# Optimization experiments

Measured on AMD Instinct MI355X. Metric: run time of the kernel, lower is better.

Reference implementation:

```python
import jax, jax.numpy as jnp
import numpy as np

SEQ_LEN = 64
WCNT = 50000
EMB = 128
TOPIC = 256
TH = TOPIC // 2          # bidirectional topic GRU hidden (num_layers=1 branch)
KCNT = 16384             # know_length
KE = 64                  # know_emb_size
SH = 512                 # seq_hidden_size
IN_S = 2 * TOPIC + 1     # 'double' score mode GRU input size


def setup_inputs() -> dict:
    key = jax.random.key(0)
    ks = jax.random.split(key, 24)
    rn = lambda k, shape, s=0.05: jax.random.normal(k, shape, jnp.float32) * s
    un = lambda k, shape: jax.random.uniform(k, shape, jnp.float32, -1.0, 1.0)

    topic = jax.random.randint(ks[0], (SEQ_LEN,), 1, WCNT)
    knowledge = jax.random.uniform(ks[1], (KCNT,), jnp.float32)
    score = jax.random.uniform(ks[2], (1,), jnp.float32)

    emb_table = rn(ks[3], (WCNT, EMB)).at[0].set(0.0)  # padding_idx=0
    # topic bidirectional GRU (torch layout: W_ih [3H, in], gates r,z,n)
    W_ih_f = rn(ks[4], (3 * TH, EMB)); W_hh_f = rn(ks[5], (3 * TH, TH))
    b_ih_f = rn(ks[6], (3 * TH,));     b_hh_f = rn(ks[7], (3 * TH,))
    W_ih_b = rn(ks[8], (3 * TH, EMB)); W_hh_b = rn(ks[9], (3 * TH, TH))
    b_ih_b = rn(ks[10], (3 * TH,));    b_hh_b = rn(ks[11], (3 * TH,))
    # knowledge embedding Linear(KCNT -> KE)
    Wk = rn(ks[12], (KE, KCNT)); bk = rn(ks[13], (KE,))
    # knowledge memory + initial hidden (uniform(-1,1) as in module)
    knowledge_memory = un(ks[14], (KCNT, KE))
    h_initial = un(ks[15], (KCNT, SH))
    # score layer Linear(TOPIC+SH -> 1)
    Ws = rn(ks[16], (1, TOPIC + SH)); bs = rn(ks[17], (1,))
    # memory-slot GRU (input IN_S, hidden SH)
    W_ih_s = rn(ks[18], (3 * SH, IN_S)); W_hh_s = rn(ks[19], (3 * SH, SH))
    b_ih_s = rn(ks[20], (3 * SH,));      b_hh_s = rn(ks[21], (3 * SH,))

    return dict(topic=topic, knowledge=knowledge, score=score, emb_table=emb_table,
                W_ih_f=W_ih_f, W_hh_f=W_hh_f, b_ih_f=b_ih_f, b_hh_f=b_hh_f,
                W_ih_b=W_ih_b, W_hh_b=W_hh_b, b_ih_b=b_ih_b, b_hh_b=b_hh_b,
                Wk=Wk, bk=bk, knowledge_memory=knowledge_memory, h_initial=h_initial,
                Ws=Ws, bs=bs, W_ih_s=W_ih_s, W_hh_s=W_hh_s, b_ih_s=b_ih_s, b_hh_s=b_hh_s)


def gru_cell(x, h, Wih, Whh, bih, bhh):
    # torch GRU cell: gates ordered (r, z, n)
    gi = x @ Wih.T + bih
    gh = h @ Whh.T + bhh
    gi_r, gi_z, gi_n = jnp.split(gi, 3, axis=-1)
    gh_r, gh_z, gh_n = jnp.split(gh, 3, axis=-1)
    r = jax.nn.sigmoid(gi_r + gh_r)
    z = jax.nn.sigmoid(gi_z + gh_z)
    n = jnp.tanh(gi_n + r * gh_n)
    return (1.0 - z) * n + z * h


def run_gru(xs, h0, Wih, Whh, bih, bhh):
    def step(h, x):
        h2 = gru_cell(x, h, Wih, Whh, bih, bhh)
        return h2, h2
    _, ys = jax.lax.scan(step, h0, xs)
    return ys


def reference(topic, knowledge, score, emb_table,
              W_ih_f, W_hh_f, b_ih_f, b_hh_f,
              W_ih_b, W_hh_b, b_ih_b, b_hh_b,
              Wk, bk, knowledge_memory, h_initial,
              Ws, bs, W_ih_s, W_hh_s, b_ih_s, b_hh_s):
    # ---- topic encoder: embedding + bidirectional GRU + max over time ----
    x = emb_table[topic]                                      # [T, EMB]
    h0 = jnp.zeros((TH,), x.dtype)
    yf = run_gru(x, h0, W_ih_f, W_hh_f, b_ih_f, b_hh_f)       # [T, TH]
    yb = run_gru(x[::-1], h0, W_ih_b, W_hh_b, b_ih_b, b_hh_b)[::-1]
    v = jnp.max(jnp.concatenate([yf, yb], axis=-1), axis=0)   # [TOPIC]

    # ---- knowledge embedding + attention over memory ----
    kn = knowledge @ Wk.T + bk                                # [KE]
    alpha = knowledge_memory @ kn                             # [KCNT]
    beta = jax.nn.softmax(alpha)                              # [KCNT]

    h = h_initial                                             # [KCNT, SH]
    hkp = beta @ h                                            # [SH] attention read
    pred_v = jnp.concatenate([v, hkp])                        # [TOPIC+SH]
    predict_score = (pred_v @ Ws[0] + bs[0]).reshape(1)       # [1]

    # ---- 'double' input construction + broadcast write to all slots ----
    pos = (score >= 0.5).astype(v.dtype)                      # [1] broadcasts over v
    x_in = jnp.concatenate([v * pos, v * (1.0 - pos), score]) # [2*TOPIC+1]
    xk = beta[:, None] * x_in[None, :]                        # [KCNT, IN_S]

    h_new = gru_cell(xk, h, W_ih_s, W_hh_s, b_ih_s, b_hh_s)   # [KCNT, SH]
    return predict_score, h_new[None]                         # ([1], [1, KCNT, SH])
```

## Files before the change

### kernel.cpp

```cpp
#include <hip/hip_runtime.h>
#include <math.h>


#define SEQ 64
#define EMB 128
#define TH 128
#define G3 384
#define KCNT 16384
#define KE 64
#define SH 512
#define GS3 1536
#define INS 513

#define N8H (KCNT * SH / 8)
#define N8W (GS3 * SH / 8)
#define NB_CVT_H 2731
#define NB_CVT_W 256
#define NB_GI 128
#define NB_KN 64
#define GRID_PREP (NB_CVT_H + NB_CVT_W + NB_GI + NB_KN)

#define SLOT_BLOCKS 512

typedef _Float16 f16x8 __attribute__((ext_vector_type(8)));
typedef float f32x4 __attribute__((ext_vector_type(4)));

__device__ __forceinline__ float sigmoidf_(float x) {
    return 1.0f / (1.0f + expf(-x));
}
__device__ __forceinline__ float sigmoid_fast(float x) {
    return 1.0f / (1.0f + __expf(-x));
}
__device__ __forceinline__ float tanh_fast(float x) {
    return 2.0f / (1.0f + __expf(-2.0f * x)) - 1.0f;
}

__device__ __forceinline__ void gl_lds16(const void* g, void* l) {
    __builtin_amdgcn_global_load_lds(
        (const __attribute__((address_space(1))) unsigned int*)g,
        (__attribute__((address_space(3))) unsigned int*)l, 16, 0, 0);
}

__global__ __launch_bounds__(384) void prep_kernel(
    const float* __restrict__ h0, _Float16* __restrict__ h16,
    const float* __restrict__ Whh_s, _Float16* __restrict__ W16,
    const int* __restrict__ topic, const float* __restrict__ emb,
    const float* __restrict__ Wih_f, const float* __restrict__ bih_f,
    const float* __restrict__ Wih_b, const float* __restrict__ bih_b,
    float* __restrict__ gi_ws,
    const float* __restrict__ Wk, const float* __restrict__ bk,
    const float* __restrict__ knowledge, float* __restrict__ kn)
{
    __shared__ float red[8];
    const int b = blockIdx.x;
    const int tid = threadIdx.x;

    if (b < NB_CVT_H + NB_CVT_W) {
        const bool isH = b < NB_CVT_H;
        const float* s = isH ? h0 : Whh_s;
        _Float16* d = isH ? h16 : W16;
        const int n8 = isH ? N8H : N8W;
        const int i = (isH ? b : b - NB_CVT_H) * 384 + tid;
        if (i < n8) {
            const float4* s4 = (const float4*)s + (size_t)i * 2;
            const float4 a = s4[0], c = s4[1];
            f16x8 o;
            o[0] = (_Float16)a.x; o[1] = (_Float16)a.y;
            o[2] = (_Float16)a.z; o[3] = (_Float16)a.w;
            o[4] = (_Float16)c.x; o[5] = (_Float16)c.y;
            o[6] = (_Float16)c.z; o[7] = (_Float16)c.w;
            *(f16x8*)(d + (size_t)i * 8) = o;
        }
        return;
    }
    if (b < NB_CVT_H + NB_CVT_W + NB_GI) {
        const int idx = b - (NB_CVT_H + NB_CVT_W);
        const int t = idx & 63;
        const int dir = idx >> 6;
        const int g = tid;
        const float* Wih = dir ? Wih_b : Wih_f;
        const float* bih = dir ? bih_b : bih_f;
        const int tok = topic[dir ? (SEQ - 1 - t) : t];
        const float4* e4 = (const float4*)(emb + (size_t)tok * EMB);
        const float4* w4 = (const float4*)(Wih + (size_t)g * EMB);
        float acc = bih[g];
        #pragma unroll
        for (int q = 0; q < EMB / 4; ++q) {
            float4 w = w4[q], e = e4[q];
            acc += w.x * e.x + w.y * e.y + w.z * e.z + w.w * e.w;
        }
        gi_ws[((size_t)dir * SEQ + t) * G3 + g] = acc;
        return;
    }
    {
        const int row = b - (NB_CVT_H + NB_CVT_W + NB_GI);
        const float4* w4 = (const float4*)(Wk + (size_t)row * KCNT);
        const float4* k4 = (const float4*)knowledge;
        float acc = 0.0f;
        for (int i = tid; i < KCNT / 4; i += 384) {
            float4 w = w4[i], k = k4[i];
            acc += w.x * k.x + w.y * k.y + w.z * k.z + w.w * k.w;
        }
        #pragma unroll
        for (int off = 32; off; off >>= 1) acc += __shfl_xor(acc, off);
        if ((tid & 63) == 0) red[tid >> 6] = acc;
        __syncthreads();
        if (tid == 0) {
            float t = bk[row];
            #pragma unroll
            for (int wv = 0; wv < 6; ++wv) t += red[wv];
            kn[row] = t;
        }
    }
}

__global__ __launch_bounds__(1024) void topic_gru_seq_kernel(
    const float* __restrict__ Whh_f, const float* __restrict__ bhh_f,
    const float* __restrict__ Whh_b, const float* __restrict__ bhh_b,
    const float* __restrict__ gi_ws, float* __restrict__ v_out)
{
    const int dir = blockIdx.x;
    const float* __restrict__ Whh = dir ? Whh_b : Whh_f;
    const float* __restrict__ bhh = dir ? bhh_b : bhh_f;
    const float* __restrict__ gi = gi_ws + (size_t)dir * SEQ * G3;
    const int tid = threadIdx.x;
    const int j = tid >> 3;
    const int s = tid & 7;

    __shared__ float gi_lds[SEQ * G3];
    __shared__ float hls[2][TH];

    {
        const float4* src = (const float4*)gi;
        float4* dst = (float4*)gi_lds;
        #pragma unroll
        for (int i = 0; i < 6; ++i)
            dst[tid + i * 1024] = src[tid + i * 1024];
    }

    float4 wr[4], wz[4], wn[4];
    {
        const float4* pr = (const float4*)(Whh + (size_t)j * TH + s * 16);
        const float4* pz = (const float4*)(Whh + (size_t)(TH + j) * TH + s * 16);
        const float4* pn = (const float4*)(Whh + (size_t)(2 * TH + j) * TH + s * 16);
        #pragma unroll
        for (int q = 0; q < 4; ++q) { wr[q] = pr[q]; wz[q] = pz[q]; wn[q] = pn[q]; }
    }
    const float bhr = bhh[j], bhz = bhh[j + TH], bhn = bhh[j + 2 * TH];

    if (tid < TH) hls[0][tid] = 0.0f;
    float h_old = 0.0f, vmax = -1e30f;
    __syncthreads();

    int cur = 0;
    for (int t = 0; t < SEQ; ++t) {
        const float4* h4 = (const float4*)(&hls[cur][s * 16]);
        float ar0 = 0.f, ar1 = 0.f, az0 = 0.f, az1 = 0.f, an0 = 0.f, an1 = 0.f;
        #pragma unroll
        for (int q = 0; q < 4; q += 2) {
            const float4 h0v = h4[q], h1v = h4[q + 1];
            ar0 = fmaf(wr[q].x, h0v.x, ar0); ar0 = fmaf(wr[q].y, h0v.y, ar0);
            ar0 = fmaf(wr[q].z, h0v.z, ar0); ar0 = fmaf(wr[q].w, h0v.w, ar0);
            ar1 = fmaf(wr[q+1].x, h1v.x, ar1); ar1 = fmaf(wr[q+1].y, h1v.y, ar1);
            ar1 = fmaf(wr[q+1].z, h1v.z, ar1); ar1 = fmaf(wr[q+1].w, h1v.w, ar1);
            az0 = fmaf(wz[q].x, h0v.x, az0); az0 = fmaf(wz[q].y, h0v.y, az0);
            az0 = fmaf(wz[q].z, h0v.z, az0); az0 = fmaf(wz[q].w, h0v.w, az0);
            az1 = fmaf(wz[q+1].x, h1v.x, az1); az1 = fmaf(wz[q+1].y, h1v.y, az1);
            az1 = fmaf(wz[q+1].z, h1v.z, az1); az1 = fmaf(wz[q+1].w, h1v.w, az1);
            an0 = fmaf(wn[q].x, h0v.x, an0); an0 = fmaf(wn[q].y, h0v.y, an0);
            an0 = fmaf(wn[q].z, h0v.z, an0); an0 = fmaf(wn[q].w, h0v.w, an0);
            an1 = fmaf(wn[q+1].x, h1v.x, an1); an1 = fmaf(wn[q+1].y, h1v.y, an1);
            an1 = fmaf(wn[q+1].z, h1v.z, an1); an1 = fmaf(wn[q+1].w, h1v.w, an1);
        }
        float ar = ar0 + ar1, az = az0 + az1, an = an0 + an1;
        ar += __shfl_xor(ar, 1); ar += __shfl_xor(ar, 2); ar += __shfl_xor(ar, 4);
        az += __shfl_xor(az, 1); az += __shfl_xor(az, 2); az += __shfl_xor(az, 4);
        an += __shfl_xor(an, 1); an += __shfl_xor(an, 2); an += __shfl_xor(an, 4);
        if (s == 0) {
            const float gir = gi_lds[t * G3 + j];
            const float giz = gi_lds[t * G3 + j + TH];
            const float gin = gi_lds[t * G3 + j + 2 * TH];
            const float r = sigmoidf_(gir + ar + bhr);
            const float z = sigmoidf_(giz + az + bhz);
            const float n = tanhf(fmaf(r, an + bhn, gin));
            const float hn = (1.0f - z) * n + z * h_old;
            hls[cur ^ 1][j] = hn;
            h_old = hn;
            vmax = fmaxf(vmax, hn);
        }
        __syncthreads();
        cur ^= 1;
    }
    if (s == 0) v_out[dir * TH + j] = vmax;
}

__global__ __launch_bounds__(256) void alpha_kernel(
    const float* __restrict__ km, const float* __restrict__ kn,
    float* __restrict__ alpha)
{
    const int idx = blockIdx.x * 256 + threadIdx.x;
    const int row = idx >> 6;
    const int lane = idx & 63;
    float p = km[(size_t)row * KE + lane] * kn[lane];
    #pragma unroll
    for (int off = 32; off; off >>= 1) p += __shfl_xor(p, off);
    if (lane == 0) alpha[row] = p;
}

__global__ __launch_bounds__(1024) void softmax_kernel(
    const float* __restrict__ alpha, float* __restrict__ beta)
{
    const int tid = threadIdx.x;
    float vals[16];
    float m = -1e30f;
    #pragma unroll
    for (int i = 0; i < 16; ++i) {
        vals[i] = alpha[tid + i * 1024];
        m = fmaxf(m, vals[i]);
    }
    #pragma unroll
    for (int off = 32; off; off >>= 1) m = fmaxf(m, __shfl_xor(m, off));
    __shared__ float red[16];
    if ((tid & 63) == 0) red[tid >> 6] = m;
    __syncthreads();
    float M = red[0];
    #pragma unroll
    for (int wv = 1; wv < 16; ++wv) M = fmaxf(M, red[wv]);
    __syncthreads();
    float s = 0.0f;
    #pragma unroll
    for (int i = 0; i < 16; ++i) {
        vals[i] = expf(vals[i] - M);
        s += vals[i];
    }
    #pragma unroll
    for (int off = 32; off; off >>= 1) s += __shfl_xor(s, off);
    if ((tid & 63) == 0) red[tid >> 6] = s;
    __syncthreads();
    float S = 0.0f;
    #pragma unroll
    for (int wv = 0; wv < 16; ++wv) S += red[wv];
    const float inv = 1.0f / S;
    #pragma unroll
    for (int i = 0; i < 16; ++i) beta[tid + i * 1024] = vals[i] * inv;
}

__global__ __launch_bounds__(512) void hkp_gih_kernel(
    const float* __restrict__ beta, const _Float16* __restrict__ h16,
    float* __restrict__ part,
    const float* __restrict__ Wih_s, const float* __restrict__ v,
    const float* __restrict__ score, float* __restrict__ g_raw)
{
    const int b = blockIdx.x;
    const int tid = threadIdx.x;
    if (b < 128) {
        const int j = tid;
        const int r0 = b * (KCNT / 128);
        float acc = 0.0f;
        for (int r = 0; r < KCNT / 128; ++r)
            acc = fmaf(beta[r0 + r], (float)h16[(size_t)(r0 + r) * SH + j], acc);
        part[(size_t)b * SH + j] = acc;
        return;
    }
    const int gid = b - 128;
    const int row = gid * 8 + (tid >> 6);
    const int lane = tid & 63;
    const float sc = score[0];
    const float pos = (sc >= 0.5f) ? 1.0f : 0.0f;
    const float om = 1.0f - pos;
    const float* wrow = Wih_s + (size_t)row * INS;
    float acc = 0.0f;
    for (int k = lane; k < INS; k += 64) {
        const float xv = (k < 256) ? v[k] * pos
                       : (k < 512) ? v[k - 256] * om : sc;
        acc = fmaf(wrow[k], xv, acc);
    }
    #pragma unroll
    for (int off = 32; off; off >>= 1) acc += __shfl_xor(acc, off);
    if (lane == 0) g_raw[row] = acc;
}

__global__ __launch_bounds__(512, 1) void slot_gru_mfma_kernel(
    const _Float16* __restrict__ h16,
    const _Float16* __restrict__ W16,
    const float* __restrict__ beta,
    const float* __restrict__ g_raw,
    const float* __restrict__ b_ih,
    const float* __restrict__ b_hh,
    const float* __restrict__ part,
    const float* __restrict__ v,
    const float* __restrict__ Ws, const float* __restrict__ bs,
    float* __restrict__ out)
{
    __shared__ _Float16 As[128 * 32];
    __shared__ _Float16 Bs[384 * 32];

    const int tid = threadIdx.x;

    if (blockIdx.x == SLOT_BLOCKS) {
        float* red = (float*)As;
        float hkp = 0.0f;
        for (int b = 0; b < 128; ++b) hkp += part[(size_t)b * SH + tid];
        float contrib = hkp * Ws[256 + tid];
        if (tid < 256) contrib += v[tid] * Ws[tid];
        #pragma unroll
        for (int off = 32; off; off >>= 1) contrib += __shfl_xor(contrib, off);
        if ((tid & 63) == 0) red[tid >> 6] = contrib;
        __syncthreads();
        if (tid == 0) {
            float p = bs[0];
            #pragma unroll
            for (int wv = 0; wv < 8; ++wv) p += red[wv];
            out[0] = p;
        }
        return;
    }

    const int lane = tid & 63;
    const int wv  = tid >> 6;
    const int wm  = (wv >> 2) * 64;
    const int wn  = (wv & 3) * 32;
    const int nt  = blockIdx.x & 3;
    const int mt  = blockIdx.x >> 2;
    const int m0  = mt * 128;
    const int c0  = nt * 128;
    const int l15 = lane & 15;
    const int l4  = lane >> 4;

    f32x4 acc[4][3][2];
    #pragma unroll
    for (int mi = 0; mi < 4; ++mi)
        #pragma unroll
        for (int g = 0; g < 3; ++g)
            #pragma unroll
            for (int ni = 0; ni < 2; ++ni)
                acc[mi][g][ni] = (f32x4){0.f, 0.f, 0.f, 0.f};

    for (int k0 = 0; k0 < SH; k0 += 32) {
        {
            const int r = tid >> 2, c = tid & 3;
            gl_lds16(h16 + (size_t)(m0 + r) * SH + k0 + c * 8, &As[tid * 8]);
        }
        #pragma unroll
        for (int p = 0; p < 3; ++p) {
            const int idx = tid + p * 512;
            const int r = idx >> 2, c = idx & 3;
            const int g = r >> 7, wcol = r & 127;
            gl_lds16(W16 + (size_t)(g * SH + c0 + wcol) * SH + k0 + c * 8,
                     &Bs[idx * 8]);
        }
        __syncthreads();

        f16x8 af[4], bf[3][2];
        #pragma unroll
        for (int mi = 0; mi < 4; ++mi)
            af[mi] = *(const f16x8*)&As[(wm + mi * 16 + l15) * 32 + l4 * 8];
        #pragma unroll
        for (int g = 0; g < 3; ++g)
            #pragma unroll
            for (int ni = 0; ni < 2; ++ni)
                bf[g][ni] = *(const f16x8*)&Bs[(g * 128 + wn + ni * 16 + l15) * 32 + l4 * 8];

        #pragma unroll
        for (int mi = 0; mi < 4; ++mi)
            #pragma unroll
            for (int g = 0; g < 3; ++g)
                #pragma unroll
                for (int ni = 0; ni < 2; ++ni)
                    acc[mi][g][ni] = __builtin_amdgcn_mfma_f32_16x16x32_f16(
                        af[mi], bf[g][ni], acc[mi][g][ni], 0, 0, 0);
        __syncthreads();
    }

    float bhh_[3][2], bih_[3][2], gr_[3][2];
    #pragma unroll
    for (int ni = 0; ni < 2; ++ni) {
        const int col = c0 + wn + ni * 16 + l15;
        #pragma unroll
        for (int g = 0; g < 3; ++g) {
            bhh_[g][ni] = b_hh[col + g * SH];
            bih_[g][ni] = b_ih[col + g * SH];
            gr_[g][ni]  = g_raw[col + g * SH];
        }
    }
    #pragma unroll
    for (int mi = 0; mi < 4; ++mi) {
        #pragma unroll
        for (int j = 0; j < 4; ++j) {
            const int row = m0 + wm + mi * 16 + l4 * 4 + j;
            const float bt = beta[row];
            #pragma unroll
            for (int ni = 0; ni < 2; ++ni) {
                const int col = c0 + wn + ni * 16 + l15;
                const float hp = (float)h16[(size_t)row * SH + col];
                const float ghr = acc[mi][0][ni][j] + bhh_[0][ni];
                const float ghz = acc[mi][1][ni][j] + bhh_[1][ni];
                const float ghn = acc[mi][2][ni][j] + bhh_[2][ni];
                const float gir = fmaf(bt, gr_[0][ni], bih_[0][ni]);
                const float giz = fmaf(bt, gr_[1][ni], bih_[1][ni]);
                const float gin = fmaf(bt, gr_[2][ni], bih_[2][ni]);
                const float r = sigmoid_fast(gir + ghr);
                const float z = sigmoid_fast(giz + ghz);
                const float n = tanh_fast(fmaf(r, ghn, gin));
                out[1 + (size_t)row * SH + col] = (1.0f - z) * n + z * hp;
            }
        }
    }
}

extern "C" void kernel_launch(void* const* d_in, const int* in_sizes, int n_in,
                              void* d_out, int out_size, void* d_ws, size_t ws_size,
                              hipStream_t stream) {
    const int*   topic     = (const int*)d_in[0];
    const float* knowledge = (const float*)d_in[1];
    const float* score     = (const float*)d_in[2];
    const float* emb       = (const float*)d_in[3];
    const float* Wih_f     = (const float*)d_in[4];
    const float* Whh_f     = (const float*)d_in[5];
    const float* bih_f     = (const float*)d_in[6];
    const float* bhh_f     = (const float*)d_in[7];
    const float* Wih_b     = (const float*)d_in[8];
    const float* Whh_b     = (const float*)d_in[9];
    const float* bih_b     = (const float*)d_in[10];
    const float* bhh_b     = (const float*)d_in[11];
    const float* Wk        = (const float*)d_in[12];
    const float* bk        = (const float*)d_in[13];
    const float* km        = (const float*)d_in[14];
    const float* h0        = (const float*)d_in[15];
    const float* Ws        = (const float*)d_in[16];
    const float* bs        = (const float*)d_in[17];
    const float* Wih_s     = (const float*)d_in[18];
    const float* Whh_s     = (const float*)d_in[19];
    const float* bih_s     = (const float*)d_in[20];
    const float* bhh_s     = (const float*)d_in[21];

    float* out = (float*)d_out;
    float* ws  = (float*)d_ws;

    float* v     = ws + 0;
    float* kn    = ws + 256;
    float* alpha = ws + 320;
    float* beta  = ws + 16704;
    float* part  = ws + 33088;
    float* g_raw = ws + 98624;
    float* gi_ws = ws + 100672;

    const size_t H16_OFF = 655360;
    const size_t W16_OFF = H16_OFF + (size_t)KCNT * SH * 2;
    _Float16* h16 = (_Float16*)((char*)d_ws + H16_OFF);
    _Float16* W16 = (_Float16*)((char*)d_ws + W16_OFF);

    prep_kernel<<<GRID_PREP, 384, 0, stream>>>(
        h0, h16, Whh_s, W16, topic, emb, Wih_f, bih_f, Wih_b, bih_b, gi_ws,
        Wk, bk, knowledge, kn);
    topic_gru_seq_kernel<<<2, 1024, 0, stream>>>(Whh_f, bhh_f, Whh_b, bhh_b,
                                                 gi_ws, v);
    alpha_kernel<<<KCNT * 64 / 256, 256, 0, stream>>>(km, kn, alpha);
    softmax_kernel<<<1, 1024, 0, stream>>>(alpha, beta);
    hkp_gih_kernel<<<320, 512, 0, stream>>>(beta, h16, part, Wih_s, v, score,
                                            g_raw);
    slot_gru_mfma_kernel<<<SLOT_BLOCKS + 1, 512, 0, stream>>>(
        h16, W16, beta, g_raw, bih_s, bhh_s, part, v, Ws, bs, out);
}
```

Baseline: 311.1 us.

## Restructure topic GRU with fp16 LDS weights and dot2, re-layout slot-GEMM LDS tiles

The sequential topic GRU now holds its recurrent weights in LDS as fp16 and computes partial dot products with packed fp16 dot2. Partial sums are reduced through shared memory instead of shuffles, and the gate math uses fast exp approximations. The slot GRU GEMM changes its LDS tile layout to k-chunk-major, which should reduce bank conflicts on the fragment reads. The trade-off is fp16 rounding of the recurrent hidden state and weights, plus an extra barrier per timestep.

```diff
diff --git a/kernel.cpp b/kernel.cpp
--- a/kernel.cpp
+++ b/kernel.cpp
@@ -23,11 +23,16 @@
 #define SLOT_BLOCKS 512
 
 typedef _Float16 f16x8 __attribute__((ext_vector_type(8)));
+typedef _Float16 f16x2 __attribute__((ext_vector_type(2)));
 typedef float f32x4 __attribute__((ext_vector_type(4)));
 
-__device__ __forceinline__ float sigmoidf_(float x) {
-    return 1.0f / (1.0f + expf(-x));
-}
+#if __has_builtin(__builtin_amdgcn_fdot2)
+#define DOT2(a, b, c) __builtin_amdgcn_fdot2((a), (b), (c), false)
+#else
+#define DOT2(a, b, c) fmaf((float)(a)[1], (float)(b)[1], \
+                           fmaf((float)(a)[0], (float)(b)[0], (c)))
+#endif
+
 __device__ __forceinline__ float sigmoid_fast(float x) {
     return 1.0f / (1.0f + __expf(-x));
 }
@@ -124,74 +129,80 @@
     const float* __restrict__ bhh = dir ? bhh_b : bhh_f;
     const float* __restrict__ gi = gi_ws + (size_t)dir * SEQ * G3;
     const int tid = threadIdx.x;
-    const int j = tid >> 3;
-    const int s = tid & 7;
-
-    __shared__ float gi_lds[SEQ * G3];
-    __shared__ float hls[2][TH];
-
-    {
-        const float4* src = (const float4*)gi;
-        float4* dst = (float4*)gi_lds;
-        #pragma unroll
-        for (int i = 0; i < 6; ++i)
-            dst[tid + i * 1024] = src[tid + i * 1024];
-    }
-
-    float4 wr[4], wz[4], wn[4];
-    {
-        const float4* pr = (const float4*)(Whh + (size_t)j * TH + s * 16);
-        const float4* pz = (const float4*)(Whh + (size_t)(TH + j) * TH + s * 16);
-        const float4* pn = (const float4*)(Whh + (size_t)(2 * TH + j) * TH + s * 16);
-        #pragma unroll
-        for (int q = 0; q < 4; ++q) { wr[q] = pr[q]; wz[q] = pz[q]; wn[q] = pn[q]; }
-    }
-    const float bhr = bhh[j], bhz = bhh[j + TH], bhn = bhh[j + 2 * TH];
-
-    if (tid < TH) hls[0][tid] = 0.0f;
+    const int j = tid & 127;
+    const int s = tid >> 7;
+
+    __shared__ _Float16 Wl[3 * 16 * TH * 8];
+    __shared__ float part[3 * TH * 9];
+    __shared__ _Float16 hls[2][TH];
+
+    #pragma unroll
+    for (int it = 0; it < 6; ++it) {
+        const int i = tid + it * 1024;
+        const int gc = i >> 7;
+        const int row = i & 127;
+        const int g = gc >> 4, c = gc & 15;
+        const float4* s4 = (const float4*)(Whh + ((size_t)(g * TH + row)) * TH + c * 8);
+        const float4 a = s4[0], bb = s4[1];
+        f16x8 o;
+        o[0] = (_Float16)a.x;  o[1] = (_Float16)a.y;
+        o[2] = (_Float16)a.z;  o[3] = (_Float16)a.w;
+        o[4] = (_Float16)bb.x; o[5] = (_Float16)bb.y;
+        o[6] = (_Float16)bb.z; o[7] = (_Float16)bb.w;
+        *(f16x8*)&Wl[(size_t)i * 8] = o;
+    }
+    if (tid < TH) hls[0][tid] = (_Float16)0.0f;
+
+    const bool gate_lane = (tid < TH);
     float h_old = 0.0f, vmax = -1e30f;
+    float bhr = 0.f, bhz = 0.f, bhn = 0.f;
+    if (gate_lane) { bhr = bhh[j]; bhz = bhh[j + TH]; bhn = bhh[j + 2 * TH]; }
     __syncthreads();
 
     int cur = 0;
     for (int t = 0; t < SEQ; ++t) {
-        const float4* h4 = (const float4*)(&hls[cur][s * 16]);
-        float ar0 = 0.f, ar1 = 0.f, az0 = 0.f, az1 = 0.f, an0 = 0.f, an1 = 0.f;
-        #pragma unroll
-        for (int q = 0; q < 4; q += 2) {
-            const float4 h0v = h4[q], h1v = h4[q + 1];
-            ar0 = fmaf(wr[q].x, h0v.x, ar0); ar0 = fmaf(wr[q].y, h0v.y, ar0);
-            ar0 = fmaf(wr[q].z, h0v.z, ar0); ar0 = fmaf(wr[q].w, h0v.w, ar0);
-            ar1 = fmaf(wr[q+1].x, h1v.x, ar1); ar1 = fmaf(wr[q+1].y, h1v.y, ar1);
-            ar1 = fmaf(wr[q+1].z, h1v.z, ar1); ar1 = fmaf(wr[q+1].w, h1v.w, ar1);
-            az0 = fmaf(wz[q].x, h0v.x, az0); az0 = fmaf(wz[q].y, h0v.y, az0);
-            az0 = fmaf(wz[q].z, h0v.z, az0); az0 = fmaf(wz[q].w, h0v.w, az0);
-            az1 = fmaf(wz[q+1].x, h1v.x, az1); az1 = fmaf(wz[q+1].y, h1v.y, az1);
-            az1 = fmaf(wz[q+1].z, h1v.z, az1); az1 = fmaf(wz[q+1].w, h1v.w, az1);
-            an0 = fmaf(wn[q].x, h0v.x, an0); an0 = fmaf(wn[q].y, h0v.y, an0);
-            an0 = fmaf(wn[q].z, h0v.z, an0); an0 = fmaf(wn[q].w, h0v.w, an0);
-            an1 = fmaf(wn[q+1].x, h1v.x, an1); an1 = fmaf(wn[q+1].y, h1v.y, an1);
-            an1 = fmaf(wn[q+1].z, h1v.z, an1); an1 = fmaf(wn[q+1].w, h1v.w, an1);
-        }
-        float ar = ar0 + ar1, az = az0 + az1, an = an0 + an1;
-        ar += __shfl_xor(ar, 1); ar += __shfl_xor(ar, 2); ar += __shfl_xor(ar, 4);
-        az += __shfl_xor(az, 1); az += __shfl_xor(az, 2); az += __shfl_xor(az, 4);
-        an += __shfl_xor(an, 1); an += __shfl_xor(an, 2); an += __shfl_xor(an, 4);
-        if (s == 0) {
-            const float gir = gi_lds[t * G3 + j];
-            const float giz = gi_lds[t * G3 + j + TH];
-            const float gin = gi_lds[t * G3 + j + 2 * TH];
-            const float r = sigmoidf_(gir + ar + bhr);
-            const float z = sigmoidf_(giz + az + bhz);
-            const float n = tanhf(fmaf(r, an + bhn, gin));
+        float gir = 0.f, giz = 0.f, gin = 0.f;
+        if (gate_lane) {
+            gir = gi[t * G3 + j];
+            giz = gi[t * G3 + j + TH];
+            gin = gi[t * G3 + j + 2 * TH];
+        }
+        union { f16x8 v; f16x2 p[4]; } hu0, hu1, wu0, wu1;
+        hu0.v = *(const f16x8*)&hls[cur][s * 16];
+        hu1.v = *(const f16x8*)&hls[cur][s * 16 + 8];
+        #pragma unroll
+        for (int g = 0; g < 3; ++g) {
+            wu0.v = *(const f16x8*)&Wl[((g * 16 + 2 * s) * TH + j) * 8];
+            wu1.v = *(const f16x8*)&Wl[((g * 16 + 2 * s + 1) * TH + j) * 8];
+            float a0 = 0.f, a1 = 0.f;
+            #pragma unroll
+            for (int e = 0; e < 4; ++e) {
+                a0 = DOT2(wu0.p[e], hu0.p[e], a0);
+                a1 = DOT2(wu1.p[e], hu1.p[e], a1);
+            }
+            part[(g * TH + j) * 9 + s] = a0 + a1;
+        }
+        __syncthreads();
+        if (gate_lane) {
+            float ar = 0.f, az = 0.f, an_ = 0.f;
+            #pragma unroll
+            for (int q = 0; q < 8; ++q) {
+                ar  += part[(0 * TH + j) * 9 + q];
+                az  += part[(1 * TH + j) * 9 + q];
+                an_ += part[(2 * TH + j) * 9 + q];
+            }
+            const float r = sigmoid_fast(gir + ar + bhr);
+            const float z = sigmoid_fast(giz + az + bhz);
+            const float n = tanh_fast(fmaf(r, an_ + bhn, gin));
             const float hn = (1.0f - z) * n + z * h_old;
-            hls[cur ^ 1][j] = hn;
+            hls[cur ^ 1][j] = (_Float16)hn;
             h_old = hn;
             vmax = fmaxf(vmax, hn);
         }
         __syncthreads();
         cur ^= 1;
     }
-    if (s == 0) v_out[dir * TH + j] = vmax;
+    if (gate_lane) v_out[dir * TH + j] = vmax;
 }
 
 __global__ __launch_bounds__(256) void alpha_kernel(
@@ -326,6 +337,8 @@
     const int c0  = nt * 128;
     const int l15 = lane & 15;
     const int l4  = lane >> 4;
+    const int sc_ = tid >> 7;
+    const int sr_ = tid & 127;
 
     f32x4 acc[4][3][2];
     #pragma unroll
@@ -337,29 +350,24 @@
                 acc[mi][g][ni] = (f32x4){0.f, 0.f, 0.f, 0.f};
 
     for (int k0 = 0; k0 < SH; k0 += 32) {
-        {
-            const int r = tid >> 2, c = tid & 3;
-            gl_lds16(h16 + (size_t)(m0 + r) * SH + k0 + c * 8, &As[tid * 8]);
-        }
+        gl_lds16(h16 + (size_t)(m0 + sr_) * SH + k0 + sc_ * 8, &As[tid * 8]);
         #pragma unroll
         for (int p = 0; p < 3; ++p) {
-            const int idx = tid + p * 512;
-            const int r = idx >> 2, c = idx & 3;
-            const int g = r >> 7, wcol = r & 127;
-            gl_lds16(W16 + (size_t)(g * SH + c0 + wcol) * SH + k0 + c * 8,
-                     &Bs[idx * 8]);
+            gl_lds16(W16 + (size_t)(p * SH + c0 + sr_) * SH + k0 + sc_ * 8,
+                     &Bs[(size_t)(tid + p * 512) * 8]);
         }
         __syncthreads();
 
         f16x8 af[4], bf[3][2];
         #pragma unroll
         for (int mi = 0; mi < 4; ++mi)
-            af[mi] = *(const f16x8*)&As[(wm + mi * 16 + l15) * 32 + l4 * 8];
+            af[mi] = *(const f16x8*)&As[(l4 * 128 + wm + mi * 16 + l15) * 8];
         #pragma unroll
         for (int g = 0; g < 3; ++g)
             #pragma unroll
             for (int ni = 0; ni < 2; ++ni)
-                bf[g][ni] = *(const f16x8*)&Bs[(g * 128 + wn + ni * 16 + l15) * 32 + l4 * 8];
+                bf[g][ni] = *(const f16x8*)
+                    &Bs[(g * 512 + l4 * 128 + wn + ni * 16 + l15) * 8];
 
         #pragma unroll
         for (int mi = 0; mi < 4; ++mi)
@@ -386,16 +394,16 @@
     #pragma unroll
     for (int mi = 0; mi < 4; ++mi) {
         #pragma unroll
-        for (int j = 0; j < 4; ++j) {
-            const int row = m0 + wm + mi * 16 + l4 * 4 + j;
+        for (int jj = 0; jj < 4; ++jj) {
+            const int row = m0 + wm + mi * 16 + l4 * 4 + jj;
             const float bt = beta[row];
             #pragma unroll
             for (int ni = 0; ni < 2; ++ni) {
                 const int col = c0 + wn + ni * 16 + l15;
                 const float hp = (float)h16[(size_t)row * SH + col];
-                const float ghr = acc[mi][0][ni][j] + bhh_[0][ni];
-                const float ghz = acc[mi][1][ni][j] + bhh_[1][ni];
-                const float ghn = acc[mi][2][ni][j] + bhh_[2][ni];
+                const float ghr = acc[mi][0][ni][jj] + bhh_[0][ni];
+                const float ghz = acc[mi][1][ni][jj] + bhh_[1][ni];
+                const float ghn = acc[mi][2][ni][jj] + bhh_[2][ni];
                 const float gir = fmaf(bt, gr_[0][ni], bih_[0][ni]);
                 const float giz = fmaf(bt, gr_[1][ni], bih_[1][ni]);
                 const float gin = fmaf(bt, gr_[2][ni], bih_[2][ni]);
```

New measurement: 304.1 us. 2.2% less time.
